# Performance work log

Measured on AMD Instinct MI355X. Metric: run time of the kernel, lower is better.

## Reference

```python
import jax, jax.numpy as jnp
import numpy as np

N_JOINTS = 24


def rotation_6d_to_matrix(d6):
    """Zhou et al. 6D -> 3x3 rotation. d6: [..., 6] -> [..., 3, 3] (rows b1,b2,b3)."""
    a1, a2 = d6[..., :3], d6[..., 3:]
    b1 = a1 / jnp.linalg.norm(a1, axis=-1, keepdims=True)
    b2 = a2 - jnp.sum(b1 * a2, axis=-1, keepdims=True) * b1
    b2 = b2 / jnp.linalg.norm(b2, axis=-1, keepdims=True)
    b3 = jnp.cross(b1, b2)
    return jnp.stack([b1, b2, b3], axis=-2)


def setup_inputs() -> dict:
    key = jax.random.key(0)
    k1, k2 = jax.random.split(key)
    N = 131072
    angles = jax.random.normal(k1, (N, N_JOINTS, 6), dtype=jnp.float32)
    xyz = jax.random.normal(k2, (1, N_JOINTS, 3), dtype=jnp.float32)
    # simple chain kinematic tree in topological order
    parent_idx = jnp.arange(0, N_JOINTS - 1, dtype=jnp.int64)
    child_idx = jnp.arange(1, N_JOINTS, dtype=jnp.int64)
    return {"angles": angles, "xyz": xyz, "parent_idx": parent_idx, "child_idx": child_idx}


def reference(angles, xyz, parent_idx, child_idx):
    rot = rotation_6d_to_matrix(angles)  # [N, J, 3, 3]
    N = rot.shape[0]
    dtype = rot.dtype
    parent = np.asarray(parent_idx)
    child = np.asarray(child_idx)
    xyz0 = xyz[0]  # [J, 3] reference skeleton
    bottom = jnp.broadcast_to(jnp.array([0.0, 0.0, 0.0, 1.0], dtype=dtype), (N, 1, 4))

    def make_m(r, t):
        # r: [N,3,3], t: [3] -> homogeneous [N,4,4] with translation r @ t
        trans = jnp.einsum('nij,j->ni', r, t)  # [N,3]
        top = jnp.concatenate([r, trans[..., None]], axis=-1)  # [N,3,4]
        return jnp.concatenate([top, bottom], axis=-2)

    M = [None] * N_JOINTS
    M[0] = make_m(rot[:, 0], xyz0[0])
    for p, c in zip(parent, child):
        p, c = int(p), int(c)
        M[c] = M[p] @ make_m(rot[:, c], xyz0[c] - xyz0[p])
    return jnp.stack(M, axis=1)[..., :3, 3]  # [N, J, 3]
```

## Files before the change

kernel.cpp:

```cpp
#include <hip/hip_runtime.h>
#include <stdint.h>


#define N_JOINTS 24
#define SPB 32
#define BT  128

#define GLOAD_LDS16(gptr, lptr)                                            \
  __builtin_amdgcn_global_load_lds(                                        \
      (const __attribute__((address_space(1))) uint32_t*)(gptr),           \
      (__attribute__((address_space(3))) uint32_t*)(lptr), 16, 0, 0)

__global__ __launch_bounds__(BT, 4) void fk_kernel(
    const float4* __restrict__ ain,
    const float*  __restrict__ xyz,
    float4* __restrict__ aout)
{
    __shared__ float4 s_buf[SPB * 36];
    __shared__ float  s_t[2][N_JOINTS * 3];

    const int tid  = threadIdx.x;
    const int w    = tid >> 6;
    const int lane = tid & 63;

    if (lane < N_JOINTS) {
        float x = xyz[lane * 3 + 0];
        float y = xyz[lane * 3 + 1];
        float z = xyz[lane * 3 + 2];
        if (lane > 0) {
            x -= xyz[lane * 3 - 3];
            y -= xyz[lane * 3 - 2];
            z -= xyz[lane * 3 - 1];
        }
        s_t[w][lane * 3 + 0] = x;
        s_t[w][lane * 3 + 1] = y;
        s_t[w][lane * 3 + 2] = z;
    }

    const size_t gbase = (size_t)blockIdx.x * (SPB * 36) + (size_t)(w * 576 + lane);
    #pragma unroll
    for (int it = 0; it < 9; ++it) {
        GLOAD_LDS16(ain + gbase + it * 64, &s_buf[w * 576 + it * 64]);
    }
    asm volatile("s_waitcnt vmcnt(0) lgkmcnt(0)" ::: "memory");
    __builtin_amdgcn_sched_barrier(0);

    const int s   = tid >> 2;
    const int seg = tid & 3;
    const float4* __restrict__ row = &s_buf[s * 36 + seg * 9];

    float R[9], t[3];
    float o[18];

    #pragma unroll
    for (int p = 0; p < 3; ++p) {
        const float4 v0 = row[p * 3 + 0];
        const float4 v1 = row[p * 3 + 1];
        const float4 v2 = row[p * 3 + 2];
        float d6[12];
        d6[0] = v0.x; d6[1] = v0.y; d6[2]  = v0.z; d6[3]  = v0.w;
        d6[4] = v1.x; d6[5] = v1.y; d6[6]  = v1.z; d6[7]  = v1.w;
        d6[8] = v2.x; d6[9] = v2.y; d6[10] = v2.z; d6[11] = v2.w;

        #pragma unroll
        for (int h = 0; h < 2; ++h) {
            const int jl = p * 2 + h;
            const int j  = seg * 6 + jl;
            const float a1x = d6[h * 6 + 0], a1y = d6[h * 6 + 1], a1z = d6[h * 6 + 2];
            const float a2x = d6[h * 6 + 3], a2y = d6[h * 6 + 4], a2z = d6[h * 6 + 5];

            const float inv1 = rsqrtf(a1x * a1x + a1y * a1y + a1z * a1z);
            const float b1x = a1x * inv1, b1y = a1y * inv1, b1z = a1z * inv1;
            const float dd = b1x * a2x + b1y * a2y + b1z * a2z;
            float b2x = a2x - dd * b1x, b2y = a2y - dd * b1y, b2z = a2z - dd * b1z;
            const float inv2 = rsqrtf(b2x * b2x + b2y * b2y + b2z * b2z);
            b2x *= inv2; b2y *= inv2; b2z *= inv2;
            const float b3x = b1y * b2z - b1z * b2y;
            const float b3y = b1z * b2x - b1x * b2z;
            const float b3z = b1x * b2y - b1y * b2x;
            const float Rj[9] = { b1x, b1y, b1z,  b2x, b2y, b2z,  b3x, b3y, b3z };

            const float tx = s_t[w][j * 3 + 0], ty = s_t[w][j * 3 + 1], tz = s_t[w][j * 3 + 2];
            const float tlx = Rj[0] * tx + Rj[1] * ty + Rj[2] * tz;
            const float tly = Rj[3] * tx + Rj[4] * ty + Rj[5] * tz;
            const float tlz = Rj[6] * tx + Rj[7] * ty + Rj[8] * tz;

            if (jl == 0) {
                #pragma unroll
                for (int k = 0; k < 9; ++k) R[k] = Rj[k];
                t[0] = tlx; t[1] = tly; t[2] = tlz;
            } else {
                t[0] += R[0] * tlx + R[1] * tly + R[2] * tlz;
                t[1] += R[3] * tlx + R[4] * tly + R[5] * tlz;
                t[2] += R[6] * tlx + R[7] * tly + R[8] * tlz;
                float Nn[9];
                #pragma unroll
                for (int r2 = 0; r2 < 3; ++r2)
                    #pragma unroll
                    for (int c = 0; c < 3; ++c)
                        Nn[r2 * 3 + c] = R[r2 * 3 + 0] * Rj[0 * 3 + c]
                                       + R[r2 * 3 + 1] * Rj[1 * 3 + c]
                                       + R[r2 * 3 + 2] * Rj[2 * 3 + c];
                #pragma unroll
                for (int k = 0; k < 9; ++k) R[k] = Nn[k];
            }
            o[jl * 3 + 0] = t[0];
            o[jl * 3 + 1] = t[1];
            o[jl * 3 + 2] = t[2];
        }
    }

    #pragma unroll
    for (int d = 1; d <= 2; d *= 2) {
        float LR[9], Lt[3];
        #pragma unroll
        for (int k = 0; k < 9; ++k) LR[k] = __shfl_up(R[k], (unsigned)d);
        #pragma unroll
        for (int c = 0; c < 3; ++c) Lt[c] = __shfl_up(t[c], (unsigned)d);
        if (seg >= d) {
            float nt0 = Lt[0] + LR[0] * t[0] + LR[1] * t[1] + LR[2] * t[2];
            float nt1 = Lt[1] + LR[3] * t[0] + LR[4] * t[1] + LR[5] * t[2];
            float nt2 = Lt[2] + LR[6] * t[0] + LR[7] * t[1] + LR[8] * t[2];
            float Nn[9];
            #pragma unroll
            for (int r2 = 0; r2 < 3; ++r2)
                #pragma unroll
                for (int c = 0; c < 3; ++c)
                    Nn[r2 * 3 + c] = LR[r2 * 3 + 0] * R[0 * 3 + c]
                                   + LR[r2 * 3 + 1] * R[1 * 3 + c]
                                   + LR[r2 * 3 + 2] * R[2 * 3 + c];
            #pragma unroll
            for (int k = 0; k < 9; ++k) R[k] = Nn[k];
            t[0] = nt0; t[1] = nt1; t[2] = nt2;
        }
    }

    float ER[9], Et[3];
    #pragma unroll
    for (int k = 0; k < 9; ++k) ER[k] = __shfl_up(R[k], 1u);
    #pragma unroll
    for (int c = 0; c < 3; ++c) Et[c] = __shfl_up(t[c], 1u);
    if (seg == 0) {
        ER[0] = 1.f; ER[1] = 0.f; ER[2] = 0.f;
        ER[3] = 0.f; ER[4] = 1.f; ER[5] = 0.f;
        ER[6] = 0.f; ER[7] = 0.f; ER[8] = 1.f;
        Et[0] = 0.f; Et[1] = 0.f; Et[2] = 0.f;
    }

    #pragma unroll
    for (int k = 0; k < 6; ++k) {
        const float ox = o[3 * k + 0], oy = o[3 * k + 1], oz = o[3 * k + 2];
        o[3 * k + 0] = Et[0] + ER[0] * ox + ER[1] * oy + ER[2] * oz;
        o[3 * k + 1] = Et[1] + ER[3] * ox + ER[4] * oy + ER[5] * oz;
        o[3 * k + 2] = Et[2] + ER[6] * ox + ER[7] * oy + ER[8] * oz;
    }

    float2* ob = reinterpret_cast<float2*>(s_buf);
    #pragma unroll
    for (int q = 0; q < 9; ++q) {
        float2 v; v.x = o[2 * q + 0]; v.y = o[2 * q + 1];
        ob[(size_t)w * 1152 + lane * 9 + q] = v;
    }

    const size_t out_base = (size_t)blockIdx.x * (SPB * 18) + (size_t)(w * 288);
    #pragma unroll
    for (int it = 0; it < 4; ++it)
        aout[out_base + lane + 64 * it] = s_buf[w * 576 + lane + 64 * it];
    if (lane < 32)
        aout[out_base + 256 + lane] = s_buf[w * 576 + 256 + lane];
}

extern "C" void kernel_launch(void* const* d_in, const int* in_sizes, int n_in,
                              void* d_out, int out_size, void* d_ws, size_t ws_size,
                              hipStream_t stream) {
    const float* angles = (const float*)d_in[0];
    const float* xyz    = (const float*)d_in[1];
    float* out = (float*)d_out;

    const int N = in_sizes[0] / (N_JOINTS * 6);
    const int grid = N / SPB;
    fk_kernel<<<grid, BT, 0, stream>>>(
        reinterpret_cast<const float4*>(angles), xyz,
        reinterpret_cast<float4*>(out));
}
```

Measured before the change: 27.27 us.

## Convert to persistent single-wave blocks with double-buffered async LDS prefetch

Replaces one-shot 128-thread blocks with a fixed grid of 2048 single-wave blocks that loop over 16-sample tiles. The next tile is prefetched into a second LDS buffer with global_load_lds while the current tile is computed, overlapping memory latency with math. The cost is fewer resident waves per CU, and no wait is placed between the LDS output staging and the later async loads that reuse that buffer, which could race.

```diff
diff --git a/kernel.cpp b/kernel.cpp
--- a/kernel.cpp
+++ b/kernel.cpp
@@ -3,25 +3,26 @@
 
 
 #define N_JOINTS 24
-#define SPB 32
-#define BT  128
+#define TS   16
+#define GRID 2048
 
 #define GLOAD_LDS16(gptr, lptr)                                            \
   __builtin_amdgcn_global_load_lds(                                        \
       (const __attribute__((address_space(1))) uint32_t*)(gptr),           \
       (__attribute__((address_space(3))) uint32_t*)(lptr), 16, 0, 0)
 
-__global__ __launch_bounds__(BT, 4) void fk_kernel(
+__global__ __launch_bounds__(64, 2) void fk_kernel(
     const float4* __restrict__ ain,
     const float*  __restrict__ xyz,
-    float4* __restrict__ aout)
+    float4* __restrict__ aout,
+    int ntiles)
 {
-    __shared__ float4 s_buf[SPB * 36];
-    __shared__ float  s_t[2][N_JOINTS * 3];
-
-    const int tid  = threadIdx.x;
-    const int w    = tid >> 6;
-    const int lane = tid & 63;
+    __shared__ float4 s_buf[2][TS * 36];
+    __shared__ float  s_t[N_JOINTS * 3];
+
+    const int lane = threadIdx.x;
+    const int s    = lane >> 2;
+    const int seg  = lane & 3;
 
     if (lane < N_JOINTS) {
         float x = xyz[lane * 3 + 0];
@@ -32,142 +33,159 @@
             y -= xyz[lane * 3 - 2];
             z -= xyz[lane * 3 - 1];
         }
-        s_t[w][lane * 3 + 0] = x;
-        s_t[w][lane * 3 + 1] = y;
-        s_t[w][lane * 3 + 2] = z;
+        s_t[lane * 3 + 0] = x;
+        s_t[lane * 3 + 1] = y;
+        s_t[lane * 3 + 2] = z;
     }
 
-    const size_t gbase = (size_t)blockIdx.x * (SPB * 36) + (size_t)(w * 576 + lane);
-    #pragma unroll
-    for (int it = 0; it < 9; ++it) {
-        GLOAD_LDS16(ain + gbase + it * 64, &s_buf[w * 576 + it * 64]);
+    int g = blockIdx.x;
+    if (g >= ntiles) return;
+
+    {
+        const size_t gb = (size_t)g * (TS * 36) + lane;
+        #pragma unroll
+        for (int it = 0; it < 9; ++it)
+            GLOAD_LDS16(ain + gb + it * 64, &s_buf[0][it * 64]);
     }
-    asm volatile("s_waitcnt vmcnt(0) lgkmcnt(0)" ::: "memory");
-    __builtin_amdgcn_sched_barrier(0);
-
-    const int s   = tid >> 2;
-    const int seg = tid & 3;
-    const float4* __restrict__ row = &s_buf[s * 36 + seg * 9];
-
-    float R[9], t[3];
-    float o[18];
-
-    #pragma unroll
-    for (int p = 0; p < 3; ++p) {
-        const float4 v0 = row[p * 3 + 0];
-        const float4 v1 = row[p * 3 + 1];
-        const float4 v2 = row[p * 3 + 2];
-        float d6[12];
-        d6[0] = v0.x; d6[1] = v0.y; d6[2]  = v0.z; d6[3]  = v0.w;
-        d6[4] = v1.x; d6[5] = v1.y; d6[6]  = v1.z; d6[7]  = v1.w;
-        d6[8] = v2.x; d6[9] = v2.y; d6[10] = v2.z; d6[11] = v2.w;
-
-        #pragma unroll
-        for (int h = 0; h < 2; ++h) {
-            const int jl = p * 2 + h;
-            const int j  = seg * 6 + jl;
-            const float a1x = d6[h * 6 + 0], a1y = d6[h * 6 + 1], a1z = d6[h * 6 + 2];
-            const float a2x = d6[h * 6 + 3], a2y = d6[h * 6 + 4], a2z = d6[h * 6 + 5];
-
-            const float inv1 = rsqrtf(a1x * a1x + a1y * a1y + a1z * a1z);
-            const float b1x = a1x * inv1, b1y = a1y * inv1, b1z = a1z * inv1;
-            const float dd = b1x * a2x + b1y * a2y + b1z * a2z;
-            float b2x = a2x - dd * b1x, b2y = a2y - dd * b1y, b2z = a2z - dd * b1z;
-            const float inv2 = rsqrtf(b2x * b2x + b2y * b2y + b2z * b2z);
-            b2x *= inv2; b2y *= inv2; b2z *= inv2;
-            const float b3x = b1y * b2z - b1z * b2y;
-            const float b3y = b1z * b2x - b1x * b2z;
-            const float b3z = b1x * b2y - b1y * b2x;
-            const float Rj[9] = { b1x, b1y, b1z,  b2x, b2y, b2z,  b3x, b3y, b3z };
-
-            const float tx = s_t[w][j * 3 + 0], ty = s_t[w][j * 3 + 1], tz = s_t[w][j * 3 + 2];
-            const float tlx = Rj[0] * tx + Rj[1] * ty + Rj[2] * tz;
-            const float tly = Rj[3] * tx + Rj[4] * ty + Rj[5] * tz;
-            const float tlz = Rj[6] * tx + Rj[7] * ty + Rj[8] * tz;
-
-            if (jl == 0) {
-                #pragma unroll
-                for (int k = 0; k < 9; ++k) R[k] = Rj[k];
-                t[0] = tlx; t[1] = tly; t[2] = tlz;
-            } else {
-                t[0] += R[0] * tlx + R[1] * tly + R[2] * tlz;
-                t[1] += R[3] * tlx + R[4] * tly + R[5] * tlz;
-                t[2] += R[6] * tlx + R[7] * tly + R[8] * tlz;
+
+    int i = 0;
+    for (; g < ntiles; g += GRID, ++i) {
+        const int cur = i & 1;
+        const int gn  = g + GRID;
+
+        if (gn < ntiles) {
+            const size_t gb = (size_t)gn * (TS * 36) + lane;
+            #pragma unroll
+            for (int it = 0; it < 9; ++it)
+                GLOAD_LDS16(ain + gb + it * 64, &s_buf[cur ^ 1][it * 64]);
+            asm volatile("s_waitcnt vmcnt(9)" ::: "memory");
+        } else {
+            asm volatile("s_waitcnt vmcnt(0)" ::: "memory");
+        }
+        __builtin_amdgcn_sched_barrier(0);
+
+        const float4* __restrict__ row = &s_buf[cur][s * 36 + seg * 9];
+
+        float R[9], t[3];
+        float o[18];
+
+        #pragma unroll
+        for (int p = 0; p < 3; ++p) {
+            const float4 v0 = row[p * 3 + 0];
+            const float4 v1 = row[p * 3 + 1];
+            const float4 v2 = row[p * 3 + 2];
+            float d6[12];
+            d6[0] = v0.x; d6[1] = v0.y; d6[2]  = v0.z; d6[3]  = v0.w;
+            d6[4] = v1.x; d6[5] = v1.y; d6[6]  = v1.z; d6[7]  = v1.w;
+            d6[8] = v2.x; d6[9] = v2.y; d6[10] = v2.z; d6[11] = v2.w;
+
+            #pragma unroll
+            for (int h = 0; h < 2; ++h) {
+                const int jl = p * 2 + h;
+                const int j  = seg * 6 + jl;
+                const float a1x = d6[h * 6 + 0], a1y = d6[h * 6 + 1], a1z = d6[h * 6 + 2];
+                const float a2x = d6[h * 6 + 3], a2y = d6[h * 6 + 4], a2z = d6[h * 6 + 5];
+
+                const float inv1 = rsqrtf(a1x * a1x + a1y * a1y + a1z * a1z);
+                const float b1x = a1x * inv1, b1y = a1y * inv1, b1z = a1z * inv1;
+                const float dd = b1x * a2x + b1y * a2y + b1z * a2z;
+                float b2x = a2x - dd * b1x, b2y = a2y - dd * b1y, b2z = a2z - dd * b1z;
+                const float inv2 = rsqrtf(b2x * b2x + b2y * b2y + b2z * b2z);
+                b2x *= inv2; b2y *= inv2; b2z *= inv2;
+                const float b3x = b1y * b2z - b1z * b2y;
+                const float b3y = b1z * b2x - b1x * b2z;
+                const float b3z = b1x * b2y - b1y * b2x;
+                const float Rj[9] = { b1x, b1y, b1z,  b2x, b2y, b2z,  b3x, b3y, b3z };
+
+                const float tx = s_t[j * 3 + 0], ty = s_t[j * 3 + 1], tz = s_t[j * 3 + 2];
+                const float tlx = Rj[0] * tx + Rj[1] * ty + Rj[2] * tz;
+                const float tly = Rj[3] * tx + Rj[4] * ty + Rj[5] * tz;
+                const float tlz = Rj[6] * tx + Rj[7] * ty + Rj[8] * tz;
+
+                if (jl == 0) {
+                    #pragma unroll
+                    for (int k = 0; k < 9; ++k) R[k] = Rj[k];
+                    t[0] = tlx; t[1] = tly; t[2] = tlz;
+                } else {
+                    t[0] += R[0] * tlx + R[1] * tly + R[2] * tlz;
+                    t[1] += R[3] * tlx + R[4] * tly + R[5] * tlz;
+                    t[2] += R[6] * tlx + R[7] * tly + R[8] * tlz;
+                    float Nn[9];
+                    #pragma unroll
+                    for (int r2 = 0; r2 < 3; ++r2)
+                        #pragma unroll
+                        for (int c = 0; c < 3; ++c)
+                            Nn[r2 * 3 + c] = R[r2 * 3 + 0] * Rj[0 * 3 + c]
+                                           + R[r2 * 3 + 1] * Rj[1 * 3 + c]
+                                           + R[r2 * 3 + 2] * Rj[2 * 3 + c];
+                    #pragma unroll
+                    for (int k = 0; k < 9; ++k) R[k] = Nn[k];
+                }
+                o[jl * 3 + 0] = t[0];
+                o[jl * 3 + 1] = t[1];
+                o[jl * 3 + 2] = t[2];
+            }
+        }
+
+        #pragma unroll
+        for (int d = 1; d <= 2; d *= 2) {
+            float LR[9], Lt[3];
+            #pragma unroll
+            for (int k = 0; k < 9; ++k) LR[k] = __shfl_up(R[k], (unsigned)d);
+            #pragma unroll
+            for (int c = 0; c < 3; ++c) Lt[c] = __shfl_up(t[c], (unsigned)d);
+            if (seg >= d) {
+                float nt0 = Lt[0] + LR[0] * t[0] + LR[1] * t[1] + LR[2] * t[2];
+                float nt1 = Lt[1] + LR[3] * t[0] + LR[4] * t[1] + LR[5] * t[2];
+                float nt2 = Lt[2] + LR[6] * t[0] + LR[7] * t[1] + LR[8] * t[2];
                 float Nn[9];
                 #pragma unroll
                 for (int r2 = 0; r2 < 3; ++r2)
                     #pragma unroll
                     for (int c = 0; c < 3; ++c)
-                        Nn[r2 * 3 + c] = R[r2 * 3 + 0] * Rj[0 * 3 + c]
-                                       + R[r2 * 3 + 1] * Rj[1 * 3 + c]
-                                       + R[r2 * 3 + 2] * Rj[2 * 3 + c];
+                        Nn[r2 * 3 + c] = LR[r2 * 3 + 0] * R[0 * 3 + c]
+                                       + LR[r2 * 3 + 1] * R[1 * 3 + c]
+                                       + LR[r2 * 3 + 2] * R[2 * 3 + c];
                 #pragma unroll
                 for (int k = 0; k < 9; ++k) R[k] = Nn[k];
+                t[0] = nt0; t[1] = nt1; t[2] = nt2;
             }
-            o[jl * 3 + 0] = t[0];
-            o[jl * 3 + 1] = t[1];
-            o[jl * 3 + 2] = t[2];
-        }
+        }
+
+        float ER[9], Et[3];
+        #pragma unroll
+        for (int k = 0; k < 9; ++k) ER[k] = __shfl_up(R[k], 1u);
+        #pragma unroll
+        for (int c = 0; c < 3; ++c) Et[c] = __shfl_up(t[c], 1u);
+        if (seg == 0) {
+            ER[0] = 1.f; ER[1] = 0.f; ER[2] = 0.f;
+            ER[3] = 0.f; ER[4] = 1.f; ER[5] = 0.f;
+            ER[6] = 0.f; ER[7] = 0.f; ER[8] = 1.f;
+            Et[0] = 0.f; Et[1] = 0.f; Et[2] = 0.f;
+        }
+
+        #pragma unroll
+        for (int k = 0; k < 6; ++k) {
+            const float ox = o[3 * k + 0], oy = o[3 * k + 1], oz = o[3 * k + 2];
+            o[3 * k + 0] = Et[0] + ER[0] * ox + ER[1] * oy + ER[2] * oz;
+            o[3 * k + 1] = Et[1] + ER[3] * ox + ER[4] * oy + ER[5] * oz;
+            o[3 * k + 2] = Et[2] + ER[6] * ox + ER[7] * oy + ER[8] * oz;
+        }
+
+        float2* ob = reinterpret_cast<float2*>(&s_buf[cur][0]);
+        #pragma unroll
+        for (int q = 0; q < 9; ++q) {
+            float2 v; v.x = o[2 * q + 0]; v.y = o[2 * q + 1];
+            ob[lane * 9 + q] = v;
+        }
+
+        const size_t out_base = (size_t)g * (TS * 18);
+        #pragma unroll
+        for (int it = 0; it < 4; ++it)
+            aout[out_base + lane + 64 * it] = s_buf[cur][lane + 64 * it];
+        if (lane < 32)
+            aout[out_base + 256 + lane] = s_buf[cur][256 + lane];
     }
-
-    #pragma unroll
-    for (int d = 1; d <= 2; d *= 2) {
-        float LR[9], Lt[3];
-        #pragma unroll
-        for (int k = 0; k < 9; ++k) LR[k] = __shfl_up(R[k], (unsigned)d);
-        #pragma unroll
-        for (int c = 0; c < 3; ++c) Lt[c] = __shfl_up(t[c], (unsigned)d);
-        if (seg >= d) {
-            float nt0 = Lt[0] + LR[0] * t[0] + LR[1] * t[1] + LR[2] * t[2];
-            float nt1 = Lt[1] + LR[3] * t[0] + LR[4] * t[1] + LR[5] * t[2];
-            float nt2 = Lt[2] + LR[6] * t[0] + LR[7] * t[1] + LR[8] * t[2];
-            float Nn[9];
-            #pragma unroll
-            for (int r2 = 0; r2 < 3; ++r2)
-                #pragma unroll
-                for (int c = 0; c < 3; ++c)
-                    Nn[r2 * 3 + c] = LR[r2 * 3 + 0] * R[0 * 3 + c]
-                                   + LR[r2 * 3 + 1] * R[1 * 3 + c]
-                                   + LR[r2 * 3 + 2] * R[2 * 3 + c];
-            #pragma unroll
-            for (int k = 0; k < 9; ++k) R[k] = Nn[k];
-            t[0] = nt0; t[1] = nt1; t[2] = nt2;
-        }
-    }
-
-    float ER[9], Et[3];
-    #pragma unroll
-    for (int k = 0; k < 9; ++k) ER[k] = __shfl_up(R[k], 1u);
-    #pragma unroll
-    for (int c = 0; c < 3; ++c) Et[c] = __shfl_up(t[c], 1u);
-    if (seg == 0) {
-        ER[0] = 1.f; ER[1] = 0.f; ER[2] = 0.f;
-        ER[3] = 0.f; ER[4] = 1.f; ER[5] = 0.f;
-        ER[6] = 0.f; ER[7] = 0.f; ER[8] = 1.f;
-        Et[0] = 0.f; Et[1] = 0.f; Et[2] = 0.f;
-    }
-
-    #pragma unroll
-    for (int k = 0; k < 6; ++k) {
-        const float ox = o[3 * k + 0], oy = o[3 * k + 1], oz = o[3 * k + 2];
-        o[3 * k + 0] = Et[0] + ER[0] * ox + ER[1] * oy + ER[2] * oz;
-        o[3 * k + 1] = Et[1] + ER[3] * ox + ER[4] * oy + ER[5] * oz;
-        o[3 * k + 2] = Et[2] + ER[6] * ox + ER[7] * oy + ER[8] * oz;
-    }
-
-    float2* ob = reinterpret_cast<float2*>(s_buf);
-    #pragma unroll
-    for (int q = 0; q < 9; ++q) {
-        float2 v; v.x = o[2 * q + 0]; v.y = o[2 * q + 1];
-        ob[(size_t)w * 1152 + lane * 9 + q] = v;
-    }
-
-    const size_t out_base = (size_t)blockIdx.x * (SPB * 18) + (size_t)(w * 288);
-    #pragma unroll
-    for (int it = 0; it < 4; ++it)
-        aout[out_base + lane + 64 * it] = s_buf[w * 576 + lane + 64 * it];
-    if (lane < 32)
-        aout[out_base + 256 + lane] = s_buf[w * 576 + 256 + lane];
 }
 
 extern "C" void kernel_launch(void* const* d_in, const int* in_sizes, int n_in,
@@ -178,8 +196,9 @@
     float* out = (float*)d_out;
 
     const int N = in_sizes[0] / (N_JOINTS * 6);
-    const int grid = N / SPB;
-    fk_kernel<<<grid, BT, 0, stream>>>(
+    const int ntiles = N / TS;
+    const int grid = (ntiles < GRID) ? ntiles : GRID;
+    fk_kernel<<<grid, 64, 0, stream>>>(
         reinterpret_cast<const float4*>(angles), xyz,
-        reinterpret_cast<float4*>(out));
+        reinterpret_cast<float4*>(out), ntiles);
 }
```

New measurement: 27.98 us. 1.03x slower.

## Split each sample's joint chain across 8 lanes instead of 4

Applied to the files above, without the earlier changes.

Each sample's 24-joint chain is now handled by 8 lanes with 3 joints each instead of 4 lanes with 6 joints. A three-step width-8 shuffle scan combines the segments, and blocks now hold 16 samples. This shortens the serial per-thread chain, lowers register use (launch bounds raised to 6 waves per SIMD), and doubles the grid size. The cost is an extra scan step, more shuffles, and scalar LDS stores for the output staging.

```diff
diff --git a/kernel.cpp b/kernel.cpp
--- a/kernel.cpp
+++ b/kernel.cpp
@@ -3,25 +3,25 @@
 
 
 #define N_JOINTS 24
-#define SPB 32
-#define BT  128
 
 #define GLOAD_LDS16(gptr, lptr)                                            \
   __builtin_amdgcn_global_load_lds(                                        \
       (const __attribute__((address_space(1))) uint32_t*)(gptr),           \
       (__attribute__((address_space(3))) uint32_t*)(lptr), 16, 0, 0)
 
-__global__ __launch_bounds__(BT, 4) void fk_kernel(
+__global__ __launch_bounds__(128, 6) void fk_kernel(
     const float4* __restrict__ ain,
     const float*  __restrict__ xyz,
     float4* __restrict__ aout)
 {
-    __shared__ float4 s_buf[SPB * 36];
+    __shared__ float4 s_buf[2][288];
     __shared__ float  s_t[2][N_JOINTS * 3];
 
     const int tid  = threadIdx.x;
     const int w    = tid >> 6;
     const int lane = tid & 63;
+    const int s    = lane >> 3;
+    const int seg  = lane & 7;
 
     if (lane < N_JOINTS) {
         float x = xyz[lane * 3 + 0];
@@ -37,98 +37,94 @@
         s_t[w][lane * 3 + 2] = z;
     }
 
-    const size_t gbase = (size_t)blockIdx.x * (SPB * 36) + (size_t)(w * 576 + lane);
-    #pragma unroll
-    for (int it = 0; it < 9; ++it) {
-        GLOAD_LDS16(ain + gbase + it * 64, &s_buf[w * 576 + it * 64]);
-    }
+    const size_t gb = (size_t)blockIdx.x * 576 + (size_t)(w * 288 + lane);
+    GLOAD_LDS16(ain + gb +   0, &s_buf[w][  0]);
+    GLOAD_LDS16(ain + gb +  64, &s_buf[w][ 64]);
+    GLOAD_LDS16(ain + gb + 128, &s_buf[w][128]);
+    GLOAD_LDS16(ain + gb + 192, &s_buf[w][192]);
+    if (lane < 32)
+        GLOAD_LDS16(ain + gb + 256, &s_buf[w][256]);
     asm volatile("s_waitcnt vmcnt(0) lgkmcnt(0)" ::: "memory");
     __builtin_amdgcn_sched_barrier(0);
 
-    const int s   = tid >> 2;
-    const int seg = tid & 3;
-    const float4* __restrict__ row = &s_buf[s * 36 + seg * 9];
+    const float2* __restrict__ inb =
+        reinterpret_cast<const float2*>(&s_buf[w][0]);
+    float2 dv[9];
+    #pragma unroll
+    for (int k = 0; k < 9; ++k)
+        dv[k] = inb[s * 72 + seg * 9 + k];
+    float d[18];
+    #pragma unroll
+    for (int k = 0; k < 9; ++k) { d[2*k] = dv[k].x; d[2*k+1] = dv[k].y; }
 
     float R[9], t[3];
-    float o[18];
+    float o[9];
 
     #pragma unroll
-    for (int p = 0; p < 3; ++p) {
-        const float4 v0 = row[p * 3 + 0];
-        const float4 v1 = row[p * 3 + 1];
-        const float4 v2 = row[p * 3 + 2];
-        float d6[12];
-        d6[0] = v0.x; d6[1] = v0.y; d6[2]  = v0.z; d6[3]  = v0.w;
-        d6[4] = v1.x; d6[5] = v1.y; d6[6]  = v1.z; d6[7]  = v1.w;
-        d6[8] = v2.x; d6[9] = v2.y; d6[10] = v2.z; d6[11] = v2.w;
+    for (int jl = 0; jl < 3; ++jl) {
+        const int j = seg * 3 + jl;
+        const float a1x = d[jl*6+0], a1y = d[jl*6+1], a1z = d[jl*6+2];
+        const float a2x = d[jl*6+3], a2y = d[jl*6+4], a2z = d[jl*6+5];
 
-        #pragma unroll
-        for (int h = 0; h < 2; ++h) {
-            const int jl = p * 2 + h;
-            const int j  = seg * 6 + jl;
-            const float a1x = d6[h * 6 + 0], a1y = d6[h * 6 + 1], a1z = d6[h * 6 + 2];
-            const float a2x = d6[h * 6 + 3], a2y = d6[h * 6 + 4], a2z = d6[h * 6 + 5];
+        const float inv1 = rsqrtf(a1x*a1x + a1y*a1y + a1z*a1z);
+        const float b1x = a1x*inv1, b1y = a1y*inv1, b1z = a1z*inv1;
+        const float dd = b1x*a2x + b1y*a2y + b1z*a2z;
+        float b2x = a2x - dd*b1x, b2y = a2y - dd*b1y, b2z = a2z - dd*b1z;
+        const float inv2 = rsqrtf(b2x*b2x + b2y*b2y + b2z*b2z);
+        b2x *= inv2; b2y *= inv2; b2z *= inv2;
+        const float b3x = b1y*b2z - b1z*b2y;
+        const float b3y = b1z*b2x - b1x*b2z;
+        const float b3z = b1x*b2y - b1y*b2x;
+        const float Rj[9] = { b1x,b1y,b1z, b2x,b2y,b2z, b3x,b3y,b3z };
 
-            const float inv1 = rsqrtf(a1x * a1x + a1y * a1y + a1z * a1z);
-            const float b1x = a1x * inv1, b1y = a1y * inv1, b1z = a1z * inv1;
-            const float dd = b1x * a2x + b1y * a2y + b1z * a2z;
-            float b2x = a2x - dd * b1x, b2y = a2y - dd * b1y, b2z = a2z - dd * b1z;
-            const float inv2 = rsqrtf(b2x * b2x + b2y * b2y + b2z * b2z);
-            b2x *= inv2; b2y *= inv2; b2z *= inv2;
-            const float b3x = b1y * b2z - b1z * b2y;
-            const float b3y = b1z * b2x - b1x * b2z;
-            const float b3z = b1x * b2y - b1y * b2x;
-            const float Rj[9] = { b1x, b1y, b1z,  b2x, b2y, b2z,  b3x, b3y, b3z };
+        const float tx = s_t[w][j*3+0], ty = s_t[w][j*3+1], tz = s_t[w][j*3+2];
+        const float tlx = Rj[0]*tx + Rj[1]*ty + Rj[2]*tz;
+        const float tly = Rj[3]*tx + Rj[4]*ty + Rj[5]*tz;
+        const float tlz = Rj[6]*tx + Rj[7]*ty + Rj[8]*tz;
 
-            const float tx = s_t[w][j * 3 + 0], ty = s_t[w][j * 3 + 1], tz = s_t[w][j * 3 + 2];
-            const float tlx = Rj[0] * tx + Rj[1] * ty + Rj[2] * tz;
-            const float tly = Rj[3] * tx + Rj[4] * ty + Rj[5] * tz;
-            const float tlz = Rj[6] * tx + Rj[7] * ty + Rj[8] * tz;
-
-            if (jl == 0) {
-                #pragma unroll
-                for (int k = 0; k < 9; ++k) R[k] = Rj[k];
-                t[0] = tlx; t[1] = tly; t[2] = tlz;
-            } else {
-                t[0] += R[0] * tlx + R[1] * tly + R[2] * tlz;
-                t[1] += R[3] * tlx + R[4] * tly + R[5] * tlz;
-                t[2] += R[6] * tlx + R[7] * tly + R[8] * tlz;
-                float Nn[9];
-                #pragma unroll
-                for (int r2 = 0; r2 < 3; ++r2)
-                    #pragma unroll
-                    for (int c = 0; c < 3; ++c)
-                        Nn[r2 * 3 + c] = R[r2 * 3 + 0] * Rj[0 * 3 + c]
-                                       + R[r2 * 3 + 1] * Rj[1 * 3 + c]
-                                       + R[r2 * 3 + 2] * Rj[2 * 3 + c];
-                #pragma unroll
-                for (int k = 0; k < 9; ++k) R[k] = Nn[k];
-            }
-            o[jl * 3 + 0] = t[0];
-            o[jl * 3 + 1] = t[1];
-            o[jl * 3 + 2] = t[2];
-        }
-    }
-
-    #pragma unroll
-    for (int d = 1; d <= 2; d *= 2) {
-        float LR[9], Lt[3];
-        #pragma unroll
-        for (int k = 0; k < 9; ++k) LR[k] = __shfl_up(R[k], (unsigned)d);
-        #pragma unroll
-        for (int c = 0; c < 3; ++c) Lt[c] = __shfl_up(t[c], (unsigned)d);
-        if (seg >= d) {
-            float nt0 = Lt[0] + LR[0] * t[0] + LR[1] * t[1] + LR[2] * t[2];
-            float nt1 = Lt[1] + LR[3] * t[0] + LR[4] * t[1] + LR[5] * t[2];
-            float nt2 = Lt[2] + LR[6] * t[0] + LR[7] * t[1] + LR[8] * t[2];
+        if (jl == 0) {
+            #pragma unroll
+            for (int k = 0; k < 9; ++k) R[k] = Rj[k];
+            t[0] = tlx; t[1] = tly; t[2] = tlz;
+        } else {
+            t[0] += R[0]*tlx + R[1]*tly + R[2]*tlz;
+            t[1] += R[3]*tlx + R[4]*tly + R[5]*tlz;
+            t[2] += R[6]*tlx + R[7]*tly + R[8]*tlz;
             float Nn[9];
             #pragma unroll
             for (int r2 = 0; r2 < 3; ++r2)
                 #pragma unroll
                 for (int c = 0; c < 3; ++c)
-                    Nn[r2 * 3 + c] = LR[r2 * 3 + 0] * R[0 * 3 + c]
-                                   + LR[r2 * 3 + 1] * R[1 * 3 + c]
-                                   + LR[r2 * 3 + 2] * R[2 * 3 + c];
+                    Nn[r2*3+c] = R[r2*3+0]*Rj[0*3+c]
+                               + R[r2*3+1]*Rj[1*3+c]
+                               + R[r2*3+2]*Rj[2*3+c];
+            #pragma unroll
+            for (int k = 0; k < 9; ++k) R[k] = Nn[k];
+        }
+        o[jl*3+0] = t[0];
+        o[jl*3+1] = t[1];
+        o[jl*3+2] = t[2];
+    }
+
+    #pragma unroll
+    for (int dd2 = 1; dd2 <= 4; dd2 *= 2) {
+        float LR[9], Lt[3];
+        #pragma unroll
+        for (int k = 0; k < 9; ++k) LR[k] = __shfl_up(R[k], (unsigned)dd2, 8);
+        #pragma unroll
+        for (int c = 0; c < 3; ++c) Lt[c] = __shfl_up(t[c], (unsigned)dd2, 8);
+        if (seg >= dd2) {
+            float nt0 = Lt[0] + LR[0]*t[0] + LR[1]*t[1] + LR[2]*t[2];
+            float nt1 = Lt[1] + LR[3]*t[0] + LR[4]*t[1] + LR[5]*t[2];
+            float nt2 = Lt[2] + LR[6]*t[0] + LR[7]*t[1] + LR[8]*t[2];
+            float Nn[9];
+            #pragma unroll
+            for (int r2 = 0; r2 < 3; ++r2)
+                #pragma unroll
+                for (int c = 0; c < 3; ++c)
+                    Nn[r2*3+c] = LR[r2*3+0]*R[0*3+c]
+                               + LR[r2*3+1]*R[1*3+c]
+                               + LR[r2*3+2]*R[2*3+c];
             #pragma unroll
             for (int k = 0; k < 9; ++k) R[k] = Nn[k];
             t[0] = nt0; t[1] = nt1; t[2] = nt2;
@@ -137,37 +133,34 @@
 
     float ER[9], Et[3];
     #pragma unroll
-    for (int k = 0; k < 9; ++k) ER[k] = __shfl_up(R[k], 1u);
+    for (int k = 0; k < 9; ++k) ER[k] = __shfl_up(R[k], 1u, 8);
     #pragma unroll
-    for (int c = 0; c < 3; ++c) Et[c] = __shfl_up(t[c], 1u);
+    for (int c = 0; c < 3; ++c) Et[c] = __shfl_up(t[c], 1u, 8);
     if (seg == 0) {
-        ER[0] = 1.f; ER[1] = 0.f; ER[2] = 0.f;
-        ER[3] = 0.f; ER[4] = 1.f; ER[5] = 0.f;
-        ER[6] = 0.f; ER[7] = 0.f; ER[8] = 1.f;
-        Et[0] = 0.f; Et[1] = 0.f; Et[2] = 0.f;
+        ER[0]=1.f; ER[1]=0.f; ER[2]=0.f;
+        ER[3]=0.f; ER[4]=1.f; ER[5]=0.f;
+        ER[6]=0.f; ER[7]=0.f; ER[8]=1.f;
+        Et[0]=0.f; Et[1]=0.f; Et[2]=0.f;
     }
 
     #pragma unroll
-    for (int k = 0; k < 6; ++k) {
-        const float ox = o[3 * k + 0], oy = o[3 * k + 1], oz = o[3 * k + 2];
-        o[3 * k + 0] = Et[0] + ER[0] * ox + ER[1] * oy + ER[2] * oz;
-        o[3 * k + 1] = Et[1] + ER[3] * ox + ER[4] * oy + ER[5] * oz;
-        o[3 * k + 2] = Et[2] + ER[6] * ox + ER[7] * oy + ER[8] * oz;
+    for (int k = 0; k < 3; ++k) {
+        const float ox = o[3*k+0], oy = o[3*k+1], oz = o[3*k+2];
+        o[3*k+0] = Et[0] + ER[0]*ox + ER[1]*oy + ER[2]*oz;
+        o[3*k+1] = Et[1] + ER[3]*ox + ER[4]*oy + ER[5]*oz;
+        o[3*k+2] = Et[2] + ER[6]*ox + ER[7]*oy + ER[8]*oz;
     }
 
-    float2* ob = reinterpret_cast<float2*>(s_buf);
+    float* obf = reinterpret_cast<float*>(&s_buf[w][0]);
     #pragma unroll
-    for (int q = 0; q < 9; ++q) {
-        float2 v; v.x = o[2 * q + 0]; v.y = o[2 * q + 1];
-        ob[(size_t)w * 1152 + lane * 9 + q] = v;
-    }
+    for (int i = 0; i < 9; ++i)
+        obf[s * 72 + seg * 9 + i] = o[i];
 
-    const size_t out_base = (size_t)blockIdx.x * (SPB * 18) + (size_t)(w * 288);
-    #pragma unroll
-    for (int it = 0; it < 4; ++it)
-        aout[out_base + lane + 64 * it] = s_buf[w * 576 + lane + 64 * it];
-    if (lane < 32)
-        aout[out_base + 256 + lane] = s_buf[w * 576 + 256 + lane];
+    const size_t ob4 = (size_t)blockIdx.x * 288 + (size_t)(w * 144);
+    aout[ob4 + lane]      = s_buf[w][lane];
+    aout[ob4 + 64 + lane] = s_buf[w][64 + lane];
+    if (lane < 16)
+        aout[ob4 + 128 + lane] = s_buf[w][128 + lane];
 }
 
 extern "C" void kernel_launch(void* const* d_in, const int* in_sizes, int n_in,
@@ -178,8 +171,8 @@
     float* out = (float*)d_out;
 
     const int N = in_sizes[0] / (N_JOINTS * 6);
-    const int grid = N / SPB;
-    fk_kernel<<<grid, BT, 0, stream>>>(
+    const int grid = N / 16;
+    fk_kernel<<<grid, 128, 0, stream>>>(
         reinterpret_cast<const float4*>(angles), xyz,
         reinterpret_cast<float4*>(out));
 }
```

After: 28.02 us. 2.7% more time.

## Load angles directly to registers with nontemporal loads, drop LDS input staging

Applied to the files above, without the earlier changes.

Each thread now reads its own 9 contiguous float4 values straight from global memory into registers with nontemporal loads, instead of staging the whole block's input in LDS via global_load_lds. LDS is kept only for the output transpose, which now spans the whole block and needs a __syncthreads, and the final stores are nontemporal. The aim is less LDS traffic and footprint plus streaming cache hints. The cost is that per-thread strided 144-byte loads coalesce worse across a wavefront than the old lane-contiguous staged loads.

```diff
diff --git a/kernel.cpp b/kernel.cpp
--- a/kernel.cpp
+++ b/kernel.cpp
@@ -6,18 +6,16 @@
 #define SPB 32
 #define BT  128
 
-#define GLOAD_LDS16(gptr, lptr)                                            \
-  __builtin_amdgcn_global_load_lds(                                        \
-      (const __attribute__((address_space(1))) uint32_t*)(gptr),           \
-      (__attribute__((address_space(3))) uint32_t*)(lptr), 16, 0, 0)
+typedef float v4f __attribute__((ext_vector_type(4)));
+typedef float v2f __attribute__((ext_vector_type(2)));
 
 __global__ __launch_bounds__(BT, 4) void fk_kernel(
-    const float4* __restrict__ ain,
-    const float*  __restrict__ xyz,
-    float4* __restrict__ aout)
+    const v4f* __restrict__ ain,
+    const float* __restrict__ xyz,
+    v4f* __restrict__ aout)
 {
-    __shared__ float4 s_buf[SPB * 36];
-    __shared__ float  s_t[2][N_JOINTS * 3];
+    __shared__ v4f   s_out[SPB * 18];
+    __shared__ float s_t[2][N_JOINTS * 3];
 
     const int tid  = threadIdx.x;
     const int w    = tid >> 6;
@@ -37,26 +35,22 @@
         s_t[w][lane * 3 + 2] = z;
     }
 
-    const size_t gbase = (size_t)blockIdx.x * (SPB * 36) + (size_t)(w * 576 + lane);
+    const size_t ib = (size_t)blockIdx.x * (SPB * 36) + (size_t)tid * 9;
+    v4f v[9];
     #pragma unroll
-    for (int it = 0; it < 9; ++it) {
-        GLOAD_LDS16(ain + gbase + it * 64, &s_buf[w * 576 + it * 64]);
-    }
-    asm volatile("s_waitcnt vmcnt(0) lgkmcnt(0)" ::: "memory");
-    __builtin_amdgcn_sched_barrier(0);
+    for (int k = 0; k < 9; ++k)
+        v[k] = __builtin_nontemporal_load(&ain[ib + k]);
 
-    const int s   = tid >> 2;
     const int seg = tid & 3;
-    const float4* __restrict__ row = &s_buf[s * 36 + seg * 9];
 
     float R[9], t[3];
     float o[18];
 
     #pragma unroll
     for (int p = 0; p < 3; ++p) {
-        const float4 v0 = row[p * 3 + 0];
-        const float4 v1 = row[p * 3 + 1];
-        const float4 v2 = row[p * 3 + 2];
+        const v4f v0 = v[p * 3 + 0];
+        const v4f v1 = v[p * 3 + 1];
+        const v4f v2 = v[p * 3 + 2];
         float d6[12];
         d6[0] = v0.x; d6[1] = v0.y; d6[2]  = v0.z; d6[3]  = v0.w;
         d6[4] = v1.x; d6[5] = v1.y; d6[6]  = v1.z; d6[7]  = v1.w;
@@ -80,7 +74,9 @@
             const float b3z = b1x * b2y - b1y * b2x;
             const float Rj[9] = { b1x, b1y, b1z,  b2x, b2y, b2z,  b3x, b3y, b3z };
 
-            const float tx = s_t[w][j * 3 + 0], ty = s_t[w][j * 3 + 1], tz = s_t[w][j * 3 + 2];
+            const float tx = s_t[w][j * 3 + 0];
+            const float ty = s_t[w][j * 3 + 1];
+            const float tz = s_t[w][j * 3 + 2];
             const float tlx = Rj[0] * tx + Rj[1] * ty + Rj[2] * tz;
             const float tly = Rj[3] * tx + Rj[4] * ty + Rj[5] * tz;
             const float tlz = Rj[6] * tx + Rj[7] * ty + Rj[8] * tz;
@@ -155,19 +151,22 @@
         o[3 * k + 2] = Et[2] + ER[6] * ox + ER[7] * oy + ER[8] * oz;
     }
 
-    float2* ob = reinterpret_cast<float2*>(s_buf);
+    v2f* ob = reinterpret_cast<v2f*>(s_out);
     #pragma unroll
     for (int q = 0; q < 9; ++q) {
-        float2 v; v.x = o[2 * q + 0]; v.y = o[2 * q + 1];
-        ob[(size_t)w * 1152 + lane * 9 + q] = v;
+        v2f vv; vv.x = o[2 * q + 0]; vv.y = o[2 * q + 1];
+        ob[tid * 9 + q] = vv;
     }
+    __syncthreads();
 
-    const size_t out_base = (size_t)blockIdx.x * (SPB * 18) + (size_t)(w * 288);
+    const size_t out_base = (size_t)blockIdx.x * (SPB * 18);
     #pragma unroll
     for (int it = 0; it < 4; ++it)
-        aout[out_base + lane + 64 * it] = s_buf[w * 576 + lane + 64 * it];
-    if (lane < 32)
-        aout[out_base + 256 + lane] = s_buf[w * 576 + 256 + lane];
+        __builtin_nontemporal_store(s_out[tid + BT * it],
+                                    &aout[out_base + tid + BT * it]);
+    if (tid < 64)
+        __builtin_nontemporal_store(s_out[512 + tid],
+                                    &aout[out_base + 512 + tid]);
 }
 
 extern "C" void kernel_launch(void* const* d_in, const int* in_sizes, int n_in,
@@ -180,6 +179,6 @@
     const int N = in_sizes[0] / (N_JOINTS * 6);
     const int grid = N / SPB;
     fk_kernel<<<grid, BT, 0, stream>>>(
-        reinterpret_cast<const float4*>(angles), xyz,
-        reinterpret_cast<float4*>(out));
+        reinterpret_cast<const v4f*>(angles), xyz,
+        reinterpret_cast<v4f*>(out));
 }
```

Measured after the change: 50.68 us. +85.8%, slower.
